# Performance work log

Hardware: AMD Instinct MI355X
Metric: run time of the kernel (lower is better)

## Reference

```python
import jax, jax.numpy as jnp
import numpy as np

H = 16       # num heads
HD = 64      # head dim
D = H * HD   # hidden size

def _rotate_half(x):
    x1, x2 = jnp.split(x, 2, axis=-1)
    return jnp.concatenate([-x2, x1], axis=-1)

def setup_inputs() -> dict:
    key = jax.random.key(0)
    ks = jax.random.split(key, 12)
    B, N, NP = 16, 1029, 1024  # batch, tokens (5 prefix + 1024 patches), patch tokens
    inp = {
        "hidden_states": jax.random.normal(ks[0], (B, N, D), dtype=jnp.float32),
        "sin": jax.random.uniform(ks[1], (NP, HD), dtype=jnp.float32, minval=-1.0, maxval=1.0),
        "cos": jax.random.uniform(ks[2], (NP, HD), dtype=jnp.float32, minval=-1.0, maxval=1.0),
        "Wq": jax.random.normal(ks[3], (D, D), dtype=jnp.float32) * 0.02,
        "bq": jnp.zeros((D,), dtype=jnp.float32),
        "Wk": jax.random.normal(ks[4], (D, D), dtype=jnp.float32) * 0.02,
        "bk": jnp.zeros((D,), dtype=jnp.float32),
        "Wv": jax.random.normal(ks[5], (D, D), dtype=jnp.float32) * 0.02,
        "bv": jnp.zeros((D,), dtype=jnp.float32),
        "Wo": jax.random.normal(ks[6], (D, D), dtype=jnp.float32) * 0.02,
        "bo": jnp.zeros((D,), dtype=jnp.float32),
    }
    return inp

def reference(hidden_states, sin, cos, Wq, bq, Wk, bk, Wv, bv, Wo, bo):
    B, N, _ = hidden_states.shape
    scaling = HD ** -0.5
    # qkv projections (nn.Linear: x @ W.T + b), split to heads: [B,H,N,HD]
    def proj(W, b):
        y = hidden_states @ W.T + b
        return y.reshape(B, N, H, HD).transpose(0, 2, 1, 3)
    q, k, v = proj(Wq, bq), proj(Wk, bk), proj(Wv, bv)
    # rotary pos emb on patch-token suffix only
    prefix = N - sin.shape[-2]
    def rope(x):
        xs = x[:, :, prefix:, :]
        xs = xs * cos + _rotate_half(xs) * sin
        return jnp.concatenate([x[:, :, :prefix, :], xs], axis=2)
    q, k = rope(q), rope(k)
    # eager attention: softmax in fp32
    attn = jnp.einsum("bhqd,bhkd->bhqk", q, k) * scaling
    attn = jax.nn.softmax(attn.astype(jnp.float32), axis=-1).astype(q.dtype)
    out = jnp.einsum("bhqk,bhkd->bhqd", attn, v)
    out = out.transpose(0, 2, 1, 3).reshape(B, N, D)
    return out @ Wo.T + bo
```

## Files before the change

kernel.cpp:

```cpp
#include <hip/hip_runtime.h>
#include <stdint.h>

#define H 16
#define HD 64
#define D 1024
#define NTOK 1029
#define BATCH 16
#define NPAD 1152
#define M_ROWS (BATCH*NTOK)
#define MPAD 16512
#define KB 1024
#define PREFIX 5

typedef unsigned short u16;
typedef __attribute__((ext_vector_type(8))) short short8;
typedef __attribute__((ext_vector_type(4))) short short4v;
typedef __attribute__((ext_vector_type(4))) float float4v;
typedef __attribute__((ext_vector_type(4))) unsigned int uint4v;

__device__ __forceinline__ u16 f2bf(float x) {
  unsigned int u = __float_as_uint(x);
  u += 0x7FFFu + ((u >> 16) & 1u);
  return (u16)(u >> 16);
}

__device__ __forceinline__ void gload16(const void* g, void* l) {
  __builtin_amdgcn_global_load_lds((const __attribute__((address_space(1))) void*)g,
                                   (__attribute__((address_space(3))) void*)l, 16, 0, 0);
}

__global__ __launch_bounds__(256) void cvt_A_kernel(const float* __restrict__ src,
                                                    u16* __restrict__ dst) {
  int idx = blockIdx.x * 256 + threadIdx.x;
  int m = idx >> 8, k = (idx & 255) * 4;
  float4v x = (float4v)0.f;
  if (m < M_ROWS) x = *(const float4v*)(src + (size_t)m * D + k);
  short4v o;
#pragma unroll
  for (int j = 0; j < 4; j++) o[j] = (short)f2bf(x[j]);
  *(short4v*)(dst + (size_t)m * D + k) = o;
}

__global__ __launch_bounds__(256) void cvt_W_kernel(
    const float* __restrict__ w0, const float* __restrict__ w1,
    const float* __restrict__ w2, const float* __restrict__ w3,
    u16* __restrict__ e0, u16* __restrict__ e1, u16* __restrict__ e2, u16* __restrict__ e3) {
  const float* src = (blockIdx.y == 0) ? w0 : (blockIdx.y == 1) ? w1 : (blockIdx.y == 2) ? w2 : w3;
  u16* dst = (blockIdx.y == 0) ? e0 : (blockIdx.y == 1) ? e1 : (blockIdx.y == 2) ? e2 : e3;
  int idx = blockIdx.x * 256 + threadIdx.x;
  int m = idx >> 8, k = (idx & 255) * 4;
  float4v x = *(const float4v*)(src + (size_t)m * D + k);
  short4v o;
#pragma unroll
  for (int j = 0; j < 4; j++) o[j] = (short)f2bf(x[j]);
  *(short4v*)(dst + (size_t)m * D + k) = o;
}

__device__ __forceinline__ void gemm_mainloop(const u16* __restrict__ A,
                                              const u16* __restrict__ Bw,
                                              u16* As, u16* Bs, int mtile, int ntile,
                                              float4v acc[4][4]) {
  const int tid = threadIdx.x;
  const int lane = tid & 63;
  const int wave = tid >> 6;
  const int wm = (wave >> 1) * 64;
  const int wn = (wave & 1) * 64;
  const int ar = lane & 15;
  const int kq = lane >> 4;
#pragma unroll
  for (int i = 0; i < 4; i++)
#pragma unroll
    for (int j = 0; j < 4; j++) acc[i][j] = (float4v)0.f;

  const size_t abase = (size_t)mtile * 128 * KB;
  const size_t bbase = (size_t)ntile * 128 * KB;
  for (int k0 = 0; k0 < KB; k0 += 32) {
    __syncthreads();
#pragma unroll
    for (int i = 0; i < 2; i++) {
      int chunk = i * 256 + tid;
      gload16(A + abase + (size_t)(chunk >> 2) * KB + k0 + (chunk & 3) * 8,
              As + (size_t)(i * 256 + (tid & ~63)) * 8);
      gload16(Bw + bbase + (size_t)(chunk >> 2) * KB + k0 + (chunk & 3) * 8,
              Bs + (size_t)(i * 256 + (tid & ~63)) * 8);
    }
    __syncthreads();
    short8 af[4], bf[4];
#pragma unroll
    for (int ms = 0; ms < 4; ms++)
      af[ms] = *(const short8*)(As + (wm + ms * 16 + ar) * 32 + kq * 8);
#pragma unroll
    for (int ns = 0; ns < 4; ns++)
      bf[ns] = *(const short8*)(Bs + (wn + ns * 16 + ar) * 32 + kq * 8);
#pragma unroll
    for (int ms = 0; ms < 4; ms++)
#pragma unroll
      for (int ns = 0; ns < 4; ns++)
        acc[ms][ns] = __builtin_amdgcn_mfma_f32_16x16x32_bf16(af[ms], bf[ns], acc[ms][ns], 0, 0, 0);
  }
}

__global__ __launch_bounds__(256) void gemm_qkv_kernel(
    const u16* __restrict__ A,
    const u16* __restrict__ Wqb, const u16* __restrict__ Wkb, const u16* __restrict__ Wvb,
    const float* __restrict__ bq, const float* __restrict__ bk, const float* __restrict__ bv,
    const float* __restrict__ sinp, const float* __restrict__ cosp,
    u16* __restrict__ qb, u16* __restrict__ kb, u16* __restrict__ vt) {
  __shared__ __align__(16) u16 As[128 * 32];
  __shared__ __align__(16) u16 Bs[128 * 32];
  const int z = blockIdx.z;
  const u16* Bw = (z == 0) ? Wqb : (z == 1) ? Wkb : Wvb;
  const float* bias = (z == 0) ? bq : (z == 1) ? bk : bv;
  const int ntile = blockIdx.x, mtile = blockIdx.y;
  float4v acc[4][4];
  gemm_mainloop(A, Bw, As, Bs, mtile, ntile, acc);

  const int tid = threadIdx.x, lane = tid & 63, wave = tid >> 6;
  const int wm = (wave >> 1) * 64, wn = (wave & 1) * 64;
  const int ar = lane & 15, kq = lane >> 4;
#pragma unroll
  for (int ms = 0; ms < 4; ms++) {
#pragma unroll
    for (int r = 0; r < 4; r++) {
      int grow = mtile * 128 + wm + ms * 16 + kq * 4 + r;
      if (grow >= M_ROWS) continue;
      int b = grow / NTOK;
      int n = grow - b * NTOK;
      bool dorope = (z != 2) && (n >= PREFIX);
      int pos = n - PREFIX;
#pragma unroll
      for (int ns = 0; ns < 4; ns++) {
        int col = ntile * 128 + wn + ns * 16 + ar;
        int hh = col >> 6, d = col & 63;
        float y = acc[ms][ns][r] + bias[col];
        if (z == 2) {
          vt[((size_t)(b * H + hh) * 64 + d) * NPAD + n] = f2bf(y);
          continue;
        }
        if (dorope) {
          float xp = acc[ms][ns ^ 2][r] + bias[col ^ 32];
          float c = cosp[pos * HD + d], s = sinp[pos * HD + d];
          y = y * c + ((d < 32) ? -xp : xp) * s;
        }
        if (z == 0) y *= 0.125f;
        u16* outp = (z == 0) ? qb : kb;
        outp[((size_t)(b * H + hh) * NPAD + n) * 64 + d] = f2bf(y);
      }
    }
  }
}

#define SSHIFT 3.0f
#define NJT 17
__global__ __launch_bounds__(256) void attn_kernel(const u16* __restrict__ qb,
                                                   const u16* __restrict__ kb,
                                                   const u16* __restrict__ vt,
                                                   u16* __restrict__ ao) {
  __shared__ __align__(16) u16 sQ[128 * 72];
  __shared__ __align__(16) u16 sK[64 * 72];
  __shared__ __align__(16) u16 sV[64 * 72];
  const int tid = threadIdx.x, lane = tid & 63, wave = tid >> 6;
  const int ar = lane & 15, kq = lane >> 4;
  const int qt = blockIdx.x, hh = blockIdx.y, b = blockIdx.z;
  const int bh = b * H + hh;
  const u16* qbase = qb + (size_t)bh * NPAD * 64;
  const u16* kbase = kb + (size_t)bh * NPAD * 64;
  const u16* vbase = vt + (size_t)bh * 64 * NPAD;

#pragma unroll
  for (int i = 0; i < 4; i++) {
    int chunk = i * 256 + tid;
    int row = chunk >> 3, c = chunk & 7;
    *(uint4v*)(sQ + row * 72 + c * 8) =
        *(const uint4v*)(qbase + (size_t)(qt * 128 + row) * 64 + c * 8);
  }
  const int r0 = tid >> 3, cc = tid & 7;
  *(uint4v*)(sK + r0 * 72 + cc * 8) = *(const uint4v*)(kbase + (size_t)r0 * 64 + cc * 8);
  *(uint4v*)(sK + (32 + r0) * 72 + cc * 8) = *(const uint4v*)(kbase + (size_t)(32 + r0) * 64 + cc * 8);
  *(uint4v*)(sV + r0 * 72 + cc * 8) = *(const uint4v*)(vbase + (size_t)r0 * NPAD + cc * 8);
  *(uint4v*)(sV + (32 + r0) * 72 + cc * 8) = *(const uint4v*)(vbase + (size_t)(32 + r0) * NPAD + cc * 8);
  __syncthreads();
  short8 aq[2][2];
#pragma unroll
  for (int ms = 0; ms < 2; ms++)
#pragma unroll
    for (int ki = 0; ki < 2; ki++)
      aq[ms][ki] = *(const short8*)(sQ + (wave * 32 + ms * 16 + ar) * 72 + ki * 32 + kq * 8);
  u16* sP = sQ + wave * 32 * 72;

  float rs[2][4];
  float4v o_acc[2][4];
#pragma unroll
  for (int ms = 0; ms < 2; ms++)
#pragma unroll
    for (int r = 0; r < 4; r++) rs[ms][r] = 0.f;
#pragma unroll
  for (int ms = 0; ms < 2; ms++)
#pragma unroll
    for (int t = 0; t < 4; t++) o_acc[ms][t] = (float4v)0.f;

  for (int jt = 0; jt < NJT; jt++) {
    const bool pf = (jt + 1 < NJT);
    uint4v nk0, nk1, nv0, nv1;
    if (pf) {
      const int jn = jt + 1;
      nk0 = *(const uint4v*)(kbase + (size_t)(jn * 64 + r0) * 64 + cc * 8);
      nk1 = *(const uint4v*)(kbase + (size_t)(jn * 64 + 32 + r0) * 64 + cc * 8);
      nv0 = *(const uint4v*)(vbase + (size_t)r0 * NPAD + jn * 64 + cc * 8);
      nv1 = *(const uint4v*)(vbase + (size_t)(32 + r0) * NPAD + jn * 64 + cc * 8);
    }

    float4v s[2][4];
#pragma unroll
    for (int ms = 0; ms < 2; ms++)
#pragma unroll
      for (int t = 0; t < 4; t++) s[ms][t] = (float4v)0.f;
#pragma unroll
    for (int ki = 0; ki < 2; ki++) {
#pragma unroll
      for (int t = 0; t < 4; t++) {
        short8 bk8 = *(const short8*)(sK + (t * 16 + ar) * 72 + ki * 32 + kq * 8);
#pragma unroll
        for (int ms = 0; ms < 2; ms++)
          s[ms][t] = __builtin_amdgcn_mfma_f32_16x16x32_bf16(aq[ms][ki], bk8, s[ms][t], 0, 0, 0);
      }
    }
    if (jt == NJT - 1) {
#pragma unroll
      for (int t = 0; t < 4; t++)
        if ((NJT - 1) * 64 + t * 16 + ar >= NTOK) {
#pragma unroll
          for (int ms = 0; ms < 2; ms++) s[ms][t] = (float4v)(-INFINITY);
        }
    }
    asm volatile("" ::: "memory");
#pragma unroll
    for (int ms = 0; ms < 2; ms++)
#pragma unroll
      for (int t = 0; t < 4; t++)
#pragma unroll
        for (int r = 0; r < 4; r++) {
          float p = __expf(s[ms][t][r] - SSHIFT);
          rs[ms][r] += p;
          sP[(ms * 16 + kq * 4 + r) * 72 + t * 16 + ar] = f2bf(p);
        }
    asm volatile("" ::: "memory");
#pragma unroll
    for (int ki = 0; ki < 2; ki++) {
#pragma unroll
      for (int ms = 0; ms < 2; ms++) {
        short8 ap = *(const short8*)(sP + (ms * 16 + ar) * 72 + ki * 32 + kq * 8);
#pragma unroll
        for (int t = 0; t < 4; t++) {
          short8 bv8 = *(const short8*)(sV + (t * 16 + ar) * 72 + ki * 32 + kq * 8);
          o_acc[ms][t] = __builtin_amdgcn_mfma_f32_16x16x32_bf16(ap, bv8, o_acc[ms][t], 0, 0, 0);
        }
      }
    }
    if (pf) {
      __syncthreads();
      *(uint4v*)(sK + r0 * 72 + cc * 8) = nk0;
      *(uint4v*)(sK + (32 + r0) * 72 + cc * 8) = nk1;
      *(uint4v*)(sV + r0 * 72 + cc * 8) = nv0;
      *(uint4v*)(sV + (32 + r0) * 72 + cc * 8) = nv1;
      __syncthreads();
    }
  }
#pragma unroll
  for (int ms = 0; ms < 2; ms++)
#pragma unroll
    for (int r = 0; r < 4; r++) {
      float l = rs[ms][r];
#pragma unroll
      for (int off = 1; off < 16; off <<= 1) l += __shfl_xor(l, off, 64);
      int i = qt * 128 + wave * 32 + ms * 16 + kq * 4 + r;
      if (i >= NTOK) continue;
      float inv = 1.f / l;
      size_t mg = (size_t)b * NTOK + i;
#pragma unroll
      for (int t = 0; t < 4; t++)
        ao[mg * D + hh * 64 + t * 16 + ar] = f2bf(o_acc[ms][t][r] * inv);
    }
}

__global__ __launch_bounds__(256) void gemm_o_kernel(const u16* __restrict__ A,
                                                     const u16* __restrict__ Wob,
                                                     const float* __restrict__ bo,
                                                     float* __restrict__ out) {
  __shared__ __align__(16) u16 As[128 * 32];
  __shared__ __align__(16) u16 Bs[128 * 32];
  const int ntile = blockIdx.x, mtile = blockIdx.y;
  float4v acc[4][4];
  gemm_mainloop(A, Wob, As, Bs, mtile, ntile, acc);
  const int tid = threadIdx.x, lane = tid & 63, wave = tid >> 6;
  const int wm = (wave >> 1) * 64, wn = (wave & 1) * 64;
  const int ar = lane & 15, kq = lane >> 4;
#pragma unroll
  for (int ms = 0; ms < 4; ms++)
#pragma unroll
    for (int r = 0; r < 4; r++) {
      int grow = mtile * 128 + wm + ms * 16 + kq * 4 + r;
      if (grow >= M_ROWS) continue;
#pragma unroll
      for (int ns = 0; ns < 4; ns++) {
        int col = ntile * 128 + wn + ns * 16 + ar;
        out[(size_t)grow * D + col] = acc[ms][ns][r] + bo[col];
      }
    }
}

extern "C" void kernel_launch(void* const* d_in, const int* in_sizes, int n_in,
                              void* d_out, int out_size, void* d_ws, size_t ws_size,
                              hipStream_t stream) {
  const float* hidden = (const float*)d_in[0];
  const float* sinp = (const float*)d_in[1];
  const float* cosp = (const float*)d_in[2];
  const float* Wq = (const float*)d_in[3]; const float* bq = (const float*)d_in[4];
  const float* Wk = (const float*)d_in[5]; const float* bk = (const float*)d_in[6];
  const float* Wv = (const float*)d_in[7]; const float* bv = (const float*)d_in[8];
  const float* Wo = (const float*)d_in[9]; const float* bo = (const float*)d_in[10];
  float* out = (float*)d_out;
  (void)in_sizes; (void)n_in; (void)out_size; (void)ws_size;

  char* ws = (char*)d_ws;
  size_t off = 0;
  auto carve = [&](size_t elems) {
    u16* p = (u16*)(ws + off);
    off += ((elems * 2 + 255) & ~(size_t)255);
    return p;
  };
  u16* A_bf = carve((size_t)MPAD * KB);
  u16* Wqb = carve((size_t)D * KB);
  u16* Wkb = carve((size_t)D * KB);
  u16* Wvb = carve((size_t)D * KB);
  u16* Wob = carve((size_t)D * KB);
  u16* q_b = carve((size_t)BATCH * H * NPAD * 64);
  u16* k_b = carve((size_t)BATCH * H * NPAD * 64);
  u16* v_t = carve((size_t)BATCH * H * NPAD * 64);

  hipLaunchKernelGGL(cvt_A_kernel, dim3(MPAD), dim3(256), 0, stream, hidden, A_bf);
  hipLaunchKernelGGL(cvt_W_kernel, dim3(1024, 4), dim3(256), 0, stream,
                     Wq, Wk, Wv, Wo, Wqb, Wkb, Wvb, Wob);
  hipLaunchKernelGGL(gemm_qkv_kernel, dim3(8, 129, 3), dim3(256), 0, stream,
                     A_bf, Wqb, Wkb, Wvb, bq, bk, bv, sinp, cosp, q_b, k_b, v_t);
  hipLaunchKernelGGL(attn_kernel, dim3(9, H, BATCH), dim3(256), 0, stream, q_b, k_b, v_t, A_bf);
  hipLaunchKernelGGL(gemm_o_kernel, dim3(8, 129), dim3(256), 0, stream, A_bf, Wob, bo, out);
}
```

Before: 585.3 us.

## Double-buffer LDS tiles in GEMM mainloop to overlap global loads with MFMA

The shared GEMM mainloop used by the QKV and output projections now uses two LDS buffers per operand. The next K-slice is loaded straight to LDS while the current slice runs through MFMA, with explicit vmcnt/lgkmcnt waits and raw s_barrier calls replacing the two __syncthreads per iteration. The aim is to hide global-load latency behind compute. In exchange LDS use per block doubles to 32KB, which may lower occupancy, and correctness now depends on hand-written waitcnt counts.

```diff
diff --git a/kernel.cpp b/kernel.cpp
--- a/kernel.cpp
+++ b/kernel.cpp
@@ -56,10 +56,41 @@
   *(short4v*)(dst + (size_t)m * D + k) = o;
 }
 
+#define STAGE(dA, dB, kk)                                                    \
+  {                                                                          \
+    _Pragma("unroll") for (int i = 0; i < 2; i++) {                          \
+      int chunk = i * 256 + tid;                                             \
+      gload16(A + abase + (size_t)(chunk >> 2) * KB + (kk) + (chunk & 3) * 8,\
+              (dA) + (size_t)(i * 256 + (tid & ~63)) * 8);                   \
+      gload16(Bw + bbase + (size_t)(chunk >> 2) * KB + (kk) + (chunk & 3) * 8,\
+              (dB) + (size_t)(i * 256 + (tid & ~63)) * 8);                   \
+    }                                                                        \
+  }
+
+#define KSTEP(cA, cB, kk2, DOSTG)                                            \
+  {                                                                          \
+    short8 af[4], bf[4];                                                     \
+    _Pragma("unroll") for (int ms = 0; ms < 4; ms++)                         \
+      af[ms] = *(const short8*)((cA) + (wm + ms * 16 + ar) * 32 + kq * 8);   \
+    _Pragma("unroll") for (int ns = 0; ns < 4; ns++)                         \
+      bf[ns] = *(const short8*)((cB) + (wn + ns * 16 + ar) * 32 + kq * 8);   \
+    asm volatile("s_waitcnt lgkmcnt(0)" ::: "memory");                       \
+    __builtin_amdgcn_sched_barrier(0);                                       \
+    __builtin_amdgcn_s_barrier();          \
+    if (DOSTG) STAGE(cA, cB, kk2);            \
+    _Pragma("unroll") for (int ms = 0; ms < 4; ms++)                         \
+      _Pragma("unroll") for (int ns = 0; ns < 4; ns++)                       \
+        acc[ms][ns] = __builtin_amdgcn_mfma_f32_16x16x32_bf16(               \
+            af[ms], bf[ns], acc[ms][ns], 0, 0, 0);                           \
+    if (DOSTG) { asm volatile("s_waitcnt vmcnt(4)" ::: "memory"); }          \
+    else       { asm volatile("s_waitcnt vmcnt(0)" ::: "memory"); }          \
+    __builtin_amdgcn_s_barrier();                    \
+  }
+
 __device__ __forceinline__ void gemm_mainloop(const u16* __restrict__ A,
                                               const u16* __restrict__ Bw,
-                                              u16* As, u16* Bs, int mtile, int ntile,
-                                              float4v acc[4][4]) {
+                                              u16* As0, u16* Bs0, u16* As1, u16* Bs1,
+                                              int mtile, int ntile, float4v acc[4][4]) {
   const int tid = threadIdx.x;
   const int lane = tid & 63;
   const int wave = tid >> 6;
@@ -74,30 +105,19 @@
 
   const size_t abase = (size_t)mtile * 128 * KB;
   const size_t bbase = (size_t)ntile * 128 * KB;
-  for (int k0 = 0; k0 < KB; k0 += 32) {
-    __syncthreads();
-#pragma unroll
-    for (int i = 0; i < 2; i++) {
-      int chunk = i * 256 + tid;
-      gload16(A + abase + (size_t)(chunk >> 2) * KB + k0 + (chunk & 3) * 8,
-              As + (size_t)(i * 256 + (tid & ~63)) * 8);
-      gload16(Bw + bbase + (size_t)(chunk >> 2) * KB + k0 + (chunk & 3) * 8,
-              Bs + (size_t)(i * 256 + (tid & ~63)) * 8);
-    }
-    __syncthreads();
-    short8 af[4], bf[4];
-#pragma unroll
-    for (int ms = 0; ms < 4; ms++)
-      af[ms] = *(const short8*)(As + (wm + ms * 16 + ar) * 32 + kq * 8);
-#pragma unroll
-    for (int ns = 0; ns < 4; ns++)
-      bf[ns] = *(const short8*)(Bs + (wn + ns * 16 + ar) * 32 + kq * 8);
-#pragma unroll
-    for (int ms = 0; ms < 4; ms++)
-#pragma unroll
-      for (int ns = 0; ns < 4; ns++)
-        acc[ms][ns] = __builtin_amdgcn_mfma_f32_16x16x32_bf16(af[ms], bf[ns], acc[ms][ns], 0, 0, 0);
-  }
+
+  STAGE(As0, Bs0, 0);
+  STAGE(As1, Bs1, 32);
+  asm volatile("s_waitcnt vmcnt(4)" ::: "memory");
+  __builtin_amdgcn_s_barrier();
+
+#pragma unroll 1
+  for (int k = 0; k < 30; k += 2) {
+    KSTEP(As0, Bs0, (k + 2) * 32, 1)
+    KSTEP(As1, Bs1, (k + 3) * 32, 1)
+  }
+  KSTEP(As0, Bs0, 0, 0)
+  KSTEP(As1, Bs1, 0, 0)
 }
 
 __global__ __launch_bounds__(256) void gemm_qkv_kernel(
@@ -106,14 +126,16 @@
     const float* __restrict__ bq, const float* __restrict__ bk, const float* __restrict__ bv,
     const float* __restrict__ sinp, const float* __restrict__ cosp,
     u16* __restrict__ qb, u16* __restrict__ kb, u16* __restrict__ vt) {
-  __shared__ __align__(16) u16 As[128 * 32];
-  __shared__ __align__(16) u16 Bs[128 * 32];
+  __shared__ __align__(16) u16 As0[128 * 32];
+  __shared__ __align__(16) u16 Bs0[128 * 32];
+  __shared__ __align__(16) u16 As1[128 * 32];
+  __shared__ __align__(16) u16 Bs1[128 * 32];
   const int z = blockIdx.z;
   const u16* Bw = (z == 0) ? Wqb : (z == 1) ? Wkb : Wvb;
   const float* bias = (z == 0) ? bq : (z == 1) ? bk : bv;
   const int ntile = blockIdx.x, mtile = blockIdx.y;
   float4v acc[4][4];
-  gemm_mainloop(A, Bw, As, Bs, mtile, ntile, acc);
+  gemm_mainloop(A, Bw, As0, Bs0, As1, Bs1, mtile, ntile, acc);
 
   const int tid = threadIdx.x, lane = tid & 63, wave = tid >> 6;
   const int wm = (wave >> 1) * 64, wn = (wave & 1) * 64;
@@ -287,11 +309,13 @@
                                                      const u16* __restrict__ Wob,
                                                      const float* __restrict__ bo,
                                                      float* __restrict__ out) {
-  __shared__ __align__(16) u16 As[128 * 32];
-  __shared__ __align__(16) u16 Bs[128 * 32];
+  __shared__ __align__(16) u16 As0[128 * 32];
+  __shared__ __align__(16) u16 Bs0[128 * 32];
+  __shared__ __align__(16) u16 As1[128 * 32];
+  __shared__ __align__(16) u16 Bs1[128 * 32];
   const int ntile = blockIdx.x, mtile = blockIdx.y;
   float4v acc[4][4];
-  gemm_mainloop(A, Wob, As, Bs, mtile, ntile, acc);
+  gemm_mainloop(A, Wob, As0, Bs0, As1, Bs1, mtile, ntile, acc);
   const int tid = threadIdx.x, lane = tid & 63, wave = tid >> 6;
   const int wm = (wave >> 1) * 64, wn = (wave & 1) * 64;
   const int ar = lane & 15, kq = lane >> 4;
```

Measured after the change: 574.7 us. No clear change (-1.8%).
